# Kernel tuning notes

Measured on AMD Instinct MI355X. Metric: run time of the kernel, lower is better.

## Reference

```python
import jax, jax.numpy as jnp
import numpy as np

B, N, C = 2, 2048, 1024
H = 8
DH = C // H  # head dim = 128


def setup_inputs() -> dict:
    key = jax.random.key(0)
    ks = jax.random.split(key, 10)
    s = 1.0 / np.sqrt(C)
    return {
        "inputs_q": jax.random.normal(ks[0], (B, N, C), dtype=jnp.float32),
        "inputs_kv": jax.random.normal(ks[1], (B, N, C), dtype=jnp.float32),
        "Wq": jax.random.normal(ks[2], (C, C), dtype=jnp.float32) * s,
        "bq": jnp.zeros((C,), dtype=jnp.float32),
        "Wk": jax.random.normal(ks[3], (C, C), dtype=jnp.float32) * s,
        "bk": jnp.zeros((C,), dtype=jnp.float32),
        "Wv": jax.random.normal(ks[4], (C, C), dtype=jnp.float32) * s,
        "bv": jnp.zeros((C,), dtype=jnp.float32),
        "Wo": jax.random.normal(ks[5], (C, C), dtype=jnp.float32) * s,
        "bo": jnp.zeros((C,), dtype=jnp.float32),
    }


def reference(inputs_q, inputs_kv, Wq, bq, Wk, bk, Wv, bv, Wo, bo):
    # QKV linear projections
    q = inputs_q @ Wq + bq           # [B, N, C]
    k = inputs_kv @ Wk + bk          # [B, M, C]
    v = inputs_kv @ Wv + bv          # [B, M, C]
    # split heads
    q = q.reshape(B, N, H, DH)
    k = k.reshape(B, -1, H, DH)
    v = v.reshape(B, -1, H, DH)
    # explicit attention, matching attend(): scale by 1/sqrt(head_dim)
    attn = jnp.einsum('bnhc,bmhc->bhnm', q, k) * (1.0 / np.sqrt(DH))
    normalized = jax.nn.softmax(attn, axis=-1)  # f32 softmax (inputs are f32)
    summed = jnp.einsum('bhnm,bmhd->bnhd', normalized, v)
    summed = summed.reshape(B, N, C)  # merge heads: ...n(hd)
    # output linear
    return summed @ Wo + bo
```

## Files before the change

### kernel.cpp

```cpp
#include <hip/hip_runtime.h>

typedef unsigned short u16;
typedef __bf16 bf16;
typedef __attribute__((ext_vector_type(8))) __bf16 bf16x8;
typedef __attribute__((ext_vector_type(4))) float f32x4;

#define AS1(p) ((const __attribute__((address_space(1))) void*)(p))
#define AS3(p) ((__attribute__((address_space(3))) void*)(p))

__device__ __forceinline__ u16 f2bf(float f) {
  unsigned u = __builtin_bit_cast(unsigned, f);
  u += 0x7fffu + ((u >> 16) & 1u);
  return (u16)(u >> 16);
}

static constexpr int  B_ = 2, N_ = 2048, C_ = 1024, H_ = 8, DH_ = 128;
static constexpr long SZ_IN = (long)B_ * N_ * C_;
static constexpr long SZ_W  = (long)C_ * C_;

__global__ void k_cast(const float* __restrict__ q, const float* __restrict__ kv,
                       const float* __restrict__ W0, const float* __restrict__ W1,
                       const float* __restrict__ W2, const float* __restrict__ W3,
                       u16* __restrict__ qb, u16* __restrict__ kvb,
                       u16* __restrict__ WT)
{
  __shared__ u16 t[64][65];
  int tid = threadIdx.x;
  if (blockIdx.y < 2) {
    const float* src = blockIdx.y ? kv : q;
    u16* dst = blockIdx.y ? kvb : qb;
    long i = ((long)blockIdx.x * 256 + tid) * 8;
    float4 a = *(const float4*)(src + i);
    float4 b = *(const float4*)(src + i + 4);
    uint4 v;
    v.x = f2bf(a.x) | ((unsigned)f2bf(a.y) << 16);
    v.y = f2bf(a.z) | ((unsigned)f2bf(a.w) << 16);
    v.z = f2bf(b.x) | ((unsigned)f2bf(b.y) << 16);
    v.w = f2bf(b.z) | ((unsigned)f2bf(b.w) << 16);
    *(uint4*)(dst + i) = v;
    return;
  }
  int x = blockIdx.x;
  if (x >= 1024) return;
  int z = x >> 8, tile = x & 255;
  const float* W = (z == 0) ? W0 : (z == 1) ? W1 : (z == 2) ? W2 : W3;
  u16* dst = WT + (long)z * SZ_W;
  int n0 = (tile & 15) * 64, k0 = (tile >> 4) * 64;
#pragma unroll
  for (int r = 0; r < 4; ++r) {
    int slot = r * 256 + tid;
    int row = slot >> 4, c4 = slot & 15;
    float4 a = *(const float4*)(W + (long)(k0 + row) * 1024 + n0 + c4 * 4);
    t[c4*4+0][row] = f2bf(a.x);
    t[c4*4+1][row] = f2bf(a.y);
    t[c4*4+2][row] = f2bf(a.z);
    t[c4*4+3][row] = f2bf(a.w);
  }
  __syncthreads();
#pragma unroll
  for (int r = 0; r < 4; ++r) {
    int slot = r * 256 + tid;
    int row = slot >> 4, c4 = slot & 15;
    uint2 v;
    v.x = t[row][c4*4+0] | ((unsigned)t[row][c4*4+1] << 16);
    v.y = t[row][c4*4+2] | ((unsigned)t[row][c4*4+3] << 16);
    *(uint2*)(dst + (long)(n0 + row) * 1024 + k0 + c4 * 4) = v;
  }
}

__device__ __forceinline__ void gemm_main_128x128(
    const u16* __restrict__ A, const u16* __restrict__ BT,
    u16* lA, u16* lB, int m0, int n0, int tid, f32x4 acc[4][4])
{
  int w = tid >> 6, l = tid & 63, quad = l >> 4, lm = l & 15;
  int wm = w >> 1, wn = w & 1;
  int srow = tid >> 2, schunk = tid & 3;
  int sxw = (srow >> 1) & 3;
  int sxr = (lm >> 1) & 3;
  const u16* Ag = A + (long)(m0 + srow) * 1024 + (schunk ^ sxw) * 8;
  const u16* Bg = BT + (long)(n0 + srow) * 1024 + (schunk ^ sxw) * 8;
  u16* lAw = lA + w * 512;
  u16* lBw = lB + w * 512;
  for (int kb = 0; kb < 32; ++kb) {
    const u16* Agk = Ag + kb * 32;
    const u16* Bgk = Bg + kb * 32;
    __builtin_amdgcn_global_load_lds(AS1(Agk),           AS3(lAw),        16, 0, 0);
    __builtin_amdgcn_global_load_lds(AS1(Agk + 64*1024), AS3(lAw + 2048), 16, 0, 0);
    __builtin_amdgcn_global_load_lds(AS1(Bgk),           AS3(lBw),        16, 0, 0);
    __builtin_amdgcn_global_load_lds(AS1(Bgk + 64*1024), AS3(lBw + 2048), 16, 0, 0);
    __syncthreads();
    bf16x8 af[4], bfr[4];
#pragma unroll
    for (int mi = 0; mi < 4; ++mi)
      af[mi] = *(const bf16x8*)(lA + (wm*64 + mi*16 + lm)*32 + ((quad ^ sxr))*8);
#pragma unroll
    for (int ni = 0; ni < 4; ++ni)
      bfr[ni] = *(const bf16x8*)(lB + (wn*64 + ni*16 + lm)*32 + ((quad ^ sxr))*8);
#pragma unroll
    for (int mi = 0; mi < 4; ++mi)
#pragma unroll
      for (int ni = 0; ni < 4; ++ni)
        acc[mi][ni] = __builtin_amdgcn_mfma_f32_16x16x32_bf16(af[mi], bfr[ni], acc[mi][ni], 0, 0, 0);
    __syncthreads();
  }
}

__global__ __launch_bounds__(256, 3)
void k_gemm_qkv(const u16* __restrict__ qb, const u16* __restrict__ kvb,
                const u16* __restrict__ wt,
                const float* __restrict__ bq, const float* __restrict__ bk,
                const float* __restrict__ bv,
                u16* __restrict__ Qb, u16* __restrict__ Kb, u16* __restrict__ VTb)
{
  __shared__ u16 lA[4096], lB[4096];
  int tid = threadIdx.x;
  int z = blockIdx.z;
  f32x4 acc[4][4] = {};
  int w = tid >> 6, l = tid & 63, quad = l >> 4, lm = l & 15;
  int wm = w >> 1, wn = w & 1;

  if (z == 2) {
    int m0 = blockIdx.y * 128, n0 = blockIdx.x * 128;
    gemm_main_128x128(kvb, wt + 2 * SZ_W, lA, lB, m0, n0, tid, acc);
#pragma unroll
    for (int ni = 0; ni < 4; ++ni) {
      int n = n0 + wn*64 + ni*16 + lm;
      float bb = bv[n];
      int h = n >> 7, dd = n & 127;
#pragma unroll
      for (int mi = 0; mi < 4; ++mi) {
        int mbase = m0 + wm*64 + mi*16 + quad*4;
        int bidx = mbase >> 11, nn = mbase & 2047;
        u16 o0 = f2bf(acc[mi][ni][0] + bb), o1 = f2bf(acc[mi][ni][1] + bb);
        u16 o2 = f2bf(acc[mi][ni][2] + bb), o3 = f2bf(acc[mi][ni][3] + bb);
        uint2 v; v.x = o0 | ((unsigned)o1 << 16); v.y = o2 | ((unsigned)o3 << 16);
        *(uint2*)(VTb + ((long)(bidx*8 + h)*128 + dd)*2048 + nn) = v;
      }
    }
  } else {
    const u16* X = (z == 0) ? qb : kvb;
    const float* bias = (z == 0) ? bq : bk;
    u16* dst = (z == 0) ? Qb : Kb;
    float scale = (z == 0) ? 0.08838834764831845f : 1.0f;
    int m0 = blockIdx.x * 128, n0 = blockIdx.y * 128;
    gemm_main_128x128(wt + (long)z * SZ_W, X, lA, lB, m0, n0, tid, acc);
#pragma unroll
    for (int mi = 0; mi < 4; ++mi) {
      int chb = m0 + wm*64 + mi*16 + quad*4;
      int h = chb >> 7, d = chb & 127;
      float4 bb = *(const float4*)(bias + chb);
#pragma unroll
      for (int ni = 0; ni < 4; ++ni) {
        int tok = n0 + wn*64 + ni*16 + lm;
        int bidx = tok >> 11, nn = tok & 2047;
        u16 o0 = f2bf((acc[mi][ni][0] + bb.x) * scale);
        u16 o1 = f2bf((acc[mi][ni][1] + bb.y) * scale);
        u16 o2 = f2bf((acc[mi][ni][2] + bb.z) * scale);
        u16 o3 = f2bf((acc[mi][ni][3] + bb.w) * scale);
        uint2 v; v.x = o0 | ((unsigned)o1 << 16); v.y = o2 | ((unsigned)o3 << 16);
        *(uint2*)(dst + ((long)(bidx*8 + h)*2048 + nn)*128 + d) = v;
      }
    }
  }
}

__global__ __launch_bounds__(512, 2)
void k_attn(const u16* __restrict__ Qb, const u16* __restrict__ Kb,
            const u16* __restrict__ VTb, u16* __restrict__ Sout)
{
  __shared__ u16 smem[40960];
  u16* lP = smem + 32768;

  int tid = threadIdx.x;
  int w = tid >> 6, l = tid & 63, quad = l >> 4, lm = l & 15;
  int bh = blockIdx.x;
  int q0 = blockIdx.y * 128 + w * 16;
  const u16* Qg = Qb + ((long)bh * 2048 + q0) * 128;
  const u16* Kg = Kb + (long)bh * 2048 * 128;
  const u16* Vg = VTb + (long)bh * 128 * 2048;
  u16* lPw = lP + w * 1024;

  bf16x8 qf[4];
#pragma unroll
  for (int kk = 0; kk < 4; ++kk)
    qf[kk] = *(const bf16x8*)(Qg + (long)lm * 128 + kk*32 + quad*8);

  f32x4 accO[8] = {};
  float sumP[4] = {};

  auto stage = [&](int tt) {
    int buf = (tt & 1) * 8192;
#pragma unroll
    for (int j = 0; j < 2; ++j) {
      int s = j*512 + tid;
      int r = s >> 4, c = s & 15;
      __builtin_amdgcn_global_load_lds(
          AS1(Kg + (long)(tt*64 + r)*128 + ((c ^ (r & 7)) * 8)),
          AS3(smem + buf + (j*512 + w*64)*8), 16, 0, 0);
    }
#pragma unroll
    for (int j = 0; j < 2; ++j) {
      int s = j*512 + tid;
      int d = s >> 3, slot = s & 7;
      int c = slot ^ (d & 7);
      __builtin_amdgcn_global_load_lds(
          AS1(Vg + (long)d*2048 + tt*64 + c*8),
          AS3(smem + 16384 + buf + (j*512 + w*64)*8), 16, 0, 0);
    }
  };

  stage(0);

#pragma unroll 1
  for (int t = 0; t < 32; ++t) {
    __syncthreads();
    if (t < 31) stage(t + 1);

    const u16* bK = smem + (t & 1) * 8192;
    const u16* bV = smem + 16384 + (t & 1) * 8192;

    f32x4 accS[4] = {};
#pragma unroll
    for (int kk = 0; kk < 4; ++kk)
#pragma unroll
      for (int ni = 0; ni < 4; ++ni) {
        bf16x8 kf = *(const bf16x8*)(bK + (ni*16 + lm)*128 + (((kk*4 + quad) ^ (lm & 7)))*8);
        accS[ni] = __builtin_amdgcn_mfma_f32_16x16x32_bf16(qf[kk], kf, accS[ni], 0, 0, 0);
      }

    bf16x8 vfk[8];
#pragma unroll
    for (int ni = 0; ni < 8; ++ni)
      vfk[ni] = *(const bf16x8*)(bV + ((ni*16 + lm)*8 + ((0*4 + quad) ^ (lm & 7)))*8);

#pragma unroll
    for (int r = 0; r < 4; ++r) {
      int R = quad*4 + r;
      int xr = (quad*2 + (r >> 1)) & 3;
#pragma unroll
      for (int ni = 0; ni < 4; ++ni) {
        float p = __expf(accS[ni][r]);
        sumP[r] += p;
        int kh = ni >> 1;
        int ch = (ni & 1)*2 + (lm >> 3);
        lPw[kh*512 + (R*4 + (ch ^ xr))*8 + (lm & 7)] = f2bf(p);
      }
    }

    bf16x8 pf = *(const bf16x8*)(lPw + (lm*4 + (quad ^ ((lm >> 1) & 3)))*8);
#pragma unroll
    for (int ni = 0; ni < 8; ++ni)
      accO[ni] = __builtin_amdgcn_mfma_f32_16x16x32_bf16(pf, vfk[ni], accO[ni], 0, 0, 0);

#pragma unroll
    for (int ni = 0; ni < 8; ++ni)
      vfk[ni] = *(const bf16x8*)(bV + ((ni*16 + lm)*8 + ((1*4 + quad) ^ (lm & 7)))*8);
    pf = *(const bf16x8*)(lPw + 512 + (lm*4 + (quad ^ ((lm >> 1) & 3)))*8);
#pragma unroll
    for (int ni = 0; ni < 8; ++ni)
      accO[ni] = __builtin_amdgcn_mfma_f32_16x16x32_bf16(pf, vfk[ni], accO[ni], 0, 0, 0);
  }

  int b = bh >> 3, h = bh & 7;
#pragma unroll
  for (int r = 0; r < 4; ++r) {
    float s = sumP[r];
    s += __shfl_xor(s, 1);
    s += __shfl_xor(s, 2);
    s += __shfl_xor(s, 4);
    s += __shfl_xor(s, 8);
    float linv = 1.f / s;
#pragma unroll
    for (int ni = 0; ni < 8; ++ni) {
      float v = accO[ni][r] * linv;
      Sout[((long)(b*2048 + q0 + quad*4 + r))*1024 + h*128 + ni*16 + lm] = f2bf(v);
    }
  }
}

__global__ __launch_bounds__(256, 3)
void k_gemm_out(const u16* __restrict__ S, const u16* __restrict__ WoT,
                const float* __restrict__ bo, float* __restrict__ out)
{
  __shared__ u16 lA[4096], lB[4096];
  int tid = threadIdx.x;
  int m0 = blockIdx.x * 128, n0 = blockIdx.y * 128;
  f32x4 acc[4][4] = {};
  gemm_main_128x128(WoT, S, lA, lB, m0, n0, tid, acc);

  int w = tid >> 6, l = tid & 63, quad = l >> 4, lm = l & 15;
  int wm = w >> 1, wn = w & 1;
#pragma unroll
  for (int mi = 0; mi < 4; ++mi) {
    int chb = m0 + wm*64 + mi*16 + quad*4;
    float4 bb = *(const float4*)(bo + chb);
#pragma unroll
    for (int ni = 0; ni < 4; ++ni) {
      int tok = n0 + wn*64 + ni*16 + lm;
      float4 v;
      v.x = acc[mi][ni][0] + bb.x;
      v.y = acc[mi][ni][1] + bb.y;
      v.z = acc[mi][ni][2] + bb.z;
      v.w = acc[mi][ni][3] + bb.w;
      *(float4*)(out + (long)tok * 1024 + chb) = v;
    }
  }
}

extern "C" void kernel_launch(void* const* d_in, const int* in_sizes, int n_in,
                              void* d_out, int out_size, void* d_ws, size_t ws_size,
                              hipStream_t stream)
{
  const float* inq  = (const float*)d_in[0];
  const float* inkv = (const float*)d_in[1];
  const float* Wq = (const float*)d_in[2];
  const float* bq = (const float*)d_in[3];
  const float* Wk = (const float*)d_in[4];
  const float* bk = (const float*)d_in[5];
  const float* Wv = (const float*)d_in[6];
  const float* bv = (const float*)d_in[7];
  const float* Wo = (const float*)d_in[8];
  const float* bo = (const float*)d_in[9];

  u16* ws   = (u16*)d_ws;
  u16* ABUF = ws;
  u16* KVB  = ws + SZ_IN;
  u16* WT   = ws + 2 * SZ_IN;
  u16* Qb   = WT + 4 * SZ_W;
  u16* Kb   = Qb + SZ_IN;
  u16* VTb  = Kb + SZ_IN;

  k_cast    <<<dim3(2048, 3),   256, 0, stream>>>(inq, inkv, Wq, Wk, Wv, Wo, ABUF, KVB, WT);
  k_gemm_qkv<<<dim3(8, 32, 3),  256, 0, stream>>>(ABUF, KVB, WT, bq, bk, bv, Qb, Kb, VTb);
  k_attn    <<<dim3(16, 16),    512, 0, stream>>>(Qb, Kb, VTb, ABUF);
  k_gemm_out<<<dim3(8, 32),     256, 0, stream>>>(ABUF, WT + 3 * SZ_W, bo, (float*)d_out);
}
```

Before: 215.8 us.

## Switch attention to 32x32x16 MFMA with intra-block key split and LDS merge

Rewrites the attention kernel to use 32x32x16 bf16 MFMA tiles instead of 16x16x32. Warps are now paired: each handles 32 queries and one half of the 64 keys in every tile. The two halves' partial outputs and row sums are merged through shared memory at the end. The K swizzle and P staging layout are changed to match the new fragment shapes. The aim is fewer LDS fragment reads per FLOP and better MFMA efficiency. The cost is extra shared memory, two extra block barriers, an LDS reduction in the epilogue, and higher register pressure from 16-wide accumulators.

New measurement: 214.9 us. About the same (-0.4%).

```diff
diff --git a/kernel.cpp b/kernel.cpp
--- a/kernel.cpp
+++ b/kernel.cpp
@@ -4,6 +4,7 @@
 typedef __bf16 bf16;
 typedef __attribute__((ext_vector_type(8))) __bf16 bf16x8;
 typedef __attribute__((ext_vector_type(4))) float f32x4;
+typedef __attribute__((ext_vector_type(16))) float f32x16;
 
 #define AS1(p) ((const __attribute__((address_space(1))) void*)(p))
 #define AS3(p) ((__attribute__((address_space(3))) void*)(p))
@@ -168,44 +169,47 @@
 void k_attn(const u16* __restrict__ Qb, const u16* __restrict__ Kb,
             const u16* __restrict__ VTb, u16* __restrict__ Sout)
 {
-  __shared__ u16 smem[40960];
-  u16* lP = smem + 32768;
+  __shared__ u16 smem[43520];
+  u16*   lP    = smem + 32768;
+  float* lStat = (float*)(smem + 43008);
 
   int tid = threadIdx.x;
-  int w = tid >> 6, l = tid & 63, quad = l >> 4, lm = l & 15;
+  int w = tid >> 6, l = tid & 63;
+  int l5 = l >> 5, c31 = l & 31;
+  int qg = w >> 1, kh = w & 1;
   int bh = blockIdx.x;
-  int q0 = blockIdx.y * 128 + w * 16;
+  int q0 = blockIdx.y * 128 + qg * 32;
   const u16* Qg = Qb + ((long)bh * 2048 + q0) * 128;
   const u16* Kg = Kb + (long)bh * 2048 * 128;
   const u16* Vg = VTb + (long)bh * 128 * 2048;
-  u16* lPw = lP + w * 1024;
-
-  bf16x8 qf[4];
-#pragma unroll
-  for (int kk = 0; kk < 4; ++kk)
-    qf[kk] = *(const bf16x8*)(Qg + (long)lm * 128 + kk*32 + quad*8);
-
-  f32x4 accO[8] = {};
-  float sumP[4] = {};
+  u16* lPw = lP + w * 1280;
+
+  bf16x8 qf[8];
+#pragma unroll
+  for (int c = 0; c < 8; ++c)
+    qf[c] = *(const bf16x8*)(Qg + (long)c31 * 128 + c*16 + l5*8);
+
+  f32x16 accO[4] = {};
+  float sumP[16] = {};
 
   auto stage = [&](int tt) {
-    int buf = (tt & 1) * 8192;
+    int bufK = (tt & 1) * 8192;
+    int bufV = 16384 + (tt & 1) * 8192;
 #pragma unroll
     for (int j = 0; j < 2; ++j) {
       int s = j*512 + tid;
-      int r = s >> 4, c = s & 15;
+      int r = s >> 4, sl = s & 15;
       __builtin_amdgcn_global_load_lds(
-          AS1(Kg + (long)(tt*64 + r)*128 + ((c ^ (r & 7)) * 8)),
-          AS3(smem + buf + (j*512 + w*64)*8), 16, 0, 0);
+          AS1(Kg + (long)(tt*64 + r)*128 + ((sl ^ (r & 15)) * 8)),
+          AS3(smem + bufK + (j*512 + w*64)*8), 16, 0, 0);
     }
 #pragma unroll
     for (int j = 0; j < 2; ++j) {
       int s = j*512 + tid;
-      int d = s >> 3, slot = s & 7;
-      int c = slot ^ (d & 7);
+      int d = s >> 3, sl = s & 7;
       __builtin_amdgcn_global_load_lds(
-          AS1(Vg + (long)d*2048 + tt*64 + c*8),
-          AS3(smem + 16384 + buf + (j*512 + w*64)*8), 16, 0, 0);
+          AS1(Vg + (long)d*2048 + tt*64 + ((sl ^ (d & 7)) * 8)),
+          AS3(smem + bufV + (j*512 + w*64)*8), 16, 0, 0);
     }
   };
 
@@ -219,61 +223,71 @@
     const u16* bK = smem + (t & 1) * 8192;
     const u16* bV = smem + 16384 + (t & 1) * 8192;
 
-    f32x4 accS[4] = {};
-#pragma unroll
-    for (int kk = 0; kk < 4; ++kk)
-#pragma unroll
-      for (int ni = 0; ni < 4; ++ni) {
-        bf16x8 kf = *(const bf16x8*)(bK + (ni*16 + lm)*128 + (((kk*4 + quad) ^ (lm & 7)))*8);
-        accS[ni] = __builtin_amdgcn_mfma_f32_16x16x32_bf16(qf[kk], kf, accS[ni], 0, 0, 0);
-      }
-
-    bf16x8 vfk[8];
-#pragma unroll
-    for (int ni = 0; ni < 8; ++ni)
-      vfk[ni] = *(const bf16x8*)(bV + ((ni*16 + lm)*8 + ((0*4 + quad) ^ (lm & 7)))*8);
-
-#pragma unroll
-    for (int r = 0; r < 4; ++r) {
-      int R = quad*4 + r;
-      int xr = (quad*2 + (r >> 1)) & 3;
-#pragma unroll
-      for (int ni = 0; ni < 4; ++ni) {
-        float p = __expf(accS[ni][r]);
-        sumP[r] += p;
-        int kh = ni >> 1;
-        int ch = (ni & 1)*2 + (lm >> 3);
-        lPw[kh*512 + (R*4 + (ch ^ xr))*8 + (lm & 7)] = f2bf(p);
-      }
-    }
-
-    bf16x8 pf = *(const bf16x8*)(lPw + (lm*4 + (quad ^ ((lm >> 1) & 3)))*8);
-#pragma unroll
-    for (int ni = 0; ni < 8; ++ni)
-      accO[ni] = __builtin_amdgcn_mfma_f32_16x16x32_bf16(pf, vfk[ni], accO[ni], 0, 0, 0);
-
-#pragma unroll
-    for (int ni = 0; ni < 8; ++ni)
-      vfk[ni] = *(const bf16x8*)(bV + ((ni*16 + lm)*8 + ((1*4 + quad) ^ (lm & 7)))*8);
-    pf = *(const bf16x8*)(lPw + 512 + (lm*4 + (quad ^ ((lm >> 1) & 3)))*8);
-#pragma unroll
-    for (int ni = 0; ni < 8; ++ni)
-      accO[ni] = __builtin_amdgcn_mfma_f32_16x16x32_bf16(pf, vfk[ni], accO[ni], 0, 0, 0);
-  }
-
-  int b = bh >> 3, h = bh & 7;
-#pragma unroll
-  for (int r = 0; r < 4; ++r) {
-    float s = sumP[r];
+    f32x16 accS[2] = {};
+#pragma unroll
+    for (int c = 0; c < 8; ++c) {
+      int r = kh*32 + c31;
+      bf16x8 kf = *(const bf16x8*)(bK + (r*16 + ((2*c + l5) ^ (l & 15)))*8);
+      accS[c & 1] = __builtin_amdgcn_mfma_f32_32x32x16_bf16(qf[c], kf, accS[c & 1], 0, 0, 0);
+    }
+
+#pragma unroll
+    for (int g = 0; g < 16; ++g) {
+      int R = (g & 3) + 8*(g >> 2) + 4*l5;
+      float p = __expf(accS[0][g] + accS[1][g]);
+      sumP[g] += p;
+      lPw[R*40 + c31] = f2bf(p);
+    }
+
+#pragma unroll
+    for (int ks = 0; ks < 2; ++ks) {
+      bf16x8 pf = *(const bf16x8*)(lPw + c31*40 + ks*16 + l5*8);
+#pragma unroll
+      for (int dt = 0; dt < 4; ++dt) {
+        int d = dt*32 + c31;
+        int cc = kh*4 + ks*2 + l5;
+        bf16x8 vf = *(const bf16x8*)(bV + (d*8 + (cc ^ (d & 7)))*8);
+        accO[dt] = __builtin_amdgcn_mfma_f32_32x32x16_bf16(pf, vf, accO[dt], 0, 0, 0);
+      }
+    }
+  }
+
+#pragma unroll
+  for (int g = 0; g < 16; ++g) {
+    float s = sumP[g];
     s += __shfl_xor(s, 1);
     s += __shfl_xor(s, 2);
     s += __shfl_xor(s, 4);
     s += __shfl_xor(s, 8);
-    float linv = 1.f / s;
-#pragma unroll
-    for (int ni = 0; ni < 8; ++ni) {
-      float v = accO[ni][r] * linv;
-      Sout[((long)(b*2048 + q0 + quad*4 + r))*1024 + h*128 + ni*16 + lm] = f2bf(v);
+    s += __shfl_xor(s, 16);
+    sumP[g] = s;
+    int R = (g & 3) + 8*(g >> 2) + 4*l5;
+    lStat[(qg*2 + kh)*32 + R] = s;
+  }
+
+  float* lO = (float*)smem;
+  __syncthreads();
+  if (kh == 1) {
+#pragma unroll
+    for (int dt = 0; dt < 4; ++dt)
+#pragma unroll
+      for (int g = 0; g < 16; ++g) {
+        int R = (g & 3) + 8*(g >> 2) + 4*l5;
+        lO[(qg*32 + R)*128 + dt*32 + c31] = accO[dt][g];
+      }
+  }
+  __syncthreads();
+  if (kh == 0) {
+    int b = bh >> 3, h = bh & 7;
+#pragma unroll
+    for (int g = 0; g < 16; ++g) {
+      int R = (g & 3) + 8*(g >> 2) + 4*l5;
+      float linv = 1.f / (lStat[(qg*2)*32 + R] + lStat[(qg*2 + 1)*32 + R]);
+#pragma unroll
+      for (int dt = 0; dt < 4; ++dt) {
+        float v = (accO[dt][g] + lO[(qg*32 + R)*128 + dt*32 + c31]) * linv;
+        Sout[((long)(b*2048 + q0 + R))*1024 + h*128 + dt*32 + c31] = f2bf(v);
+      }
     }
   }
 }
```
